# Optimization experiments

Measured on AMD Instinct MI355X. Metric: run time of the kernel, lower is better.

## Reference

```python
import jax, jax.numpy as jnp
import numpy as np

THR = 1.0  # snntorch Leaky default threshold
BETA = 0.9


def setup_inputs() -> dict:
    key = jax.random.key(0)
    k_in, k_w1, k_b1, k_w2, k_b2 = jax.random.split(key, 5)
    T, B, D, H = 100, 256, 784, 256
    # binary spike train input (rate-coded)
    spike_input = (jax.random.uniform(k_in, (T, B, D)) < 0.5).astype(jnp.float32)
    # nn.Linear init: U(-1/sqrt(fan_in), 1/sqrt(fan_in))
    lim1 = 1.0 / np.sqrt(D)
    lim2 = 1.0 / np.sqrt(H)
    W1 = jax.random.uniform(k_w1, (H, D), minval=-lim1, maxval=lim1, dtype=jnp.float32)
    b1 = jax.random.uniform(k_b1, (H,), minval=-lim1, maxval=lim1, dtype=jnp.float32)
    W2 = jax.random.uniform(k_w2, (D, H), minval=-lim2, maxval=lim2, dtype=jnp.float32)
    b2 = jax.random.uniform(k_b2, (D,), minval=-lim2, maxval=lim2, dtype=jnp.float32)
    return {"spike_input": spike_input, "W1": W1, "b1": b1, "W2": W2, "b2": b2}


def _heaviside(x):
    return (x > 0).astype(x.dtype)


def reference(spike_input, W1, b1, W2, b2):
    T, B, D = spike_input.shape
    H = W1.shape[0]

    def step(carry, x_t):
        mem1, mem2 = carry
        # layer 1: Linear + Leaky LIF (reset-by-subtraction, as in snntorch)
        cur1 = x_t @ W1.T + b1                          # [B,H]
        reset1 = _heaviside(mem1 - THR)                 # spikes from previous mem
        mem1 = BETA * mem1 + cur1 - reset1 * THR
        spk1 = _heaviside(mem1 - THR)
        # layer 2
        cur2 = spk1 @ W2.T + b2                         # [B,D]
        reset2 = _heaviside(mem2 - THR)
        mem2 = BETA * mem2 + cur2 - reset2 * THR
        spk2 = _heaviside(mem2 - THR)
        return (mem1, mem2), spk2

    mem1_0 = jnp.zeros((B, H), dtype=spike_input.dtype)
    mem2_0 = jnp.zeros((B, D), dtype=spike_input.dtype)
    _, spk_out = jax.lax.scan(step, (mem1_0, mem2_0), spike_input)
    return spk_out  # [T,B,D]
```

## Files before the change

kernel.cpp:

```cpp
#include <hip/hip_runtime.h>

typedef __attribute__((ext_vector_type(8))) _Float16 f16x8;
typedef __attribute__((ext_vector_type(4))) float f32x4;

static constexpr int TT = 100, BB = 256, DD = 784, HH = 256;
static constexpr int MM = TT * BB;
static constexpr int K1PAD = 800;
static constexpr int N2PAD = 800;
static constexpr float MIDSC = 2048.0f, INVMID = 1.0f / 2048.0f;

__device__ __forceinline__ unsigned short f2h(float x) {
  _Float16 h = (_Float16)x;
  return *(unsigned short*)&h;
}
__device__ __forceinline__ float h2f(unsigned short u) {
  _Float16 h = *(_Float16*)&u;
  return (float)h;
}
__device__ __forceinline__ void glds16(const void* g, void* l) {
  __builtin_amdgcn_global_load_lds(
      (const __attribute__((address_space(1))) unsigned int*)g,
      (__attribute__((address_space(3))) unsigned int*)l, 16, 0, 0);
}

__global__ __launch_bounds__(256)
void split_w(const float* __restrict__ W, unsigned short* __restrict__ Ws,
             int N, int K, int Npad, int Kpad) {
  int idx = blockIdx.x * 256 + threadIdx.x;
  int total = Npad * Kpad;
  if (idx >= total) return;
  int row = idx / Kpad, col = idx - row * Kpad;
  float w = (row < N && col < K) ? W[row * K + col] : 0.0f;
  unsigned short h0 = f2h(w);
  float r = (w - h2f(h0)) * MIDSC;
  Ws[idx] = h0;
  Ws[total + idx] = f2h(r);
}

__global__ __launch_bounds__(256, 2)
void gemm1(const float* __restrict__ X, const unsigned short* __restrict__ Bs,
           const float* __restrict__ bias, float* __restrict__ C) {
  constexpr int Kpad = K1PAD, nkb = Kpad / 32;
  __shared__ unsigned short Asm[2][128 * 32];
  __shared__ unsigned short Bsm[3][2][128 * 32];
  const int tid = threadIdx.x;
  const int bm = blockIdx.x * 128, bn = blockIdx.y * 128;
  const int wid = tid >> 6, lane = tid & 63;
  const int wr = (wid >> 1) * 64, wc = (wid & 1) * 64;
  const int l15 = lane & 15, l4 = lane >> 4;

  f32x4 acc[2][4][4];
#pragma unroll
  for (int s = 0; s < 2; ++s)
#pragma unroll
    for (int m = 0; m < 4; ++m)
#pragma unroll
      for (int n = 0; n < 4; ++n) acc[s][m][n] = (f32x4){0.f, 0.f, 0.f, 0.f};

  const int rl = wid * 32 + (lane >> 2);
  const int ce = ((lane & 3) ^ ((lane >> 3) & 3)) * 8;
  const size_t pstr = (size_t)HH * Kpad;
  const unsigned short* bsrc0 = Bs + (size_t)(bn + rl) * Kpad + ce;
  const unsigned short* bsrc1 = Bs + (size_t)(bn + rl + 16) * Kpad + ce;

  const int rdsw = (l4 ^ ((l15 >> 1) & 3)) * 8;

  const int r0 = tid >> 2;
  const int c0log = (tid & 3) * 8;
  const int c0phys = ((tid & 3) ^ ((tid >> 3) & 3)) * 8;

  float4 aA[4], aB[4];

  auto loadA = [&](int kb, float4 (&d)[4]) {
    const int col = kb * 32 + c0log;
    const bool ok = col < DD;
    const int colc = ok ? col : 0;
    const float* p0 = &X[(size_t)(bm + r0) * DD + colc];
    const float* p1 = &X[(size_t)(bm + r0 + 64) * DD + colc];
    d[0] = *(const float4*)p0; d[1] = *(const float4*)(p0 + 4);
    d[2] = *(const float4*)p1; d[3] = *(const float4*)(p1 + 4);
    if (!ok) {
      const float4 z = make_float4(0.f, 0.f, 0.f, 0.f);
      d[0] = z; d[1] = z; d[2] = z; d[3] = z;
    }
  };
  auto packA = [&](int bi, const float4 (&s_)[4]) {
    const unsigned ONE = 0x3C00u;
    auto pk = [&](float a, float b) {
      return (a != 0.f ? ONE : 0u) | (b != 0.f ? (ONE << 16) : 0u);
    };
    uint4 v0, v1;
    v0.x = pk(s_[0].x, s_[0].y); v0.y = pk(s_[0].z, s_[0].w);
    v0.z = pk(s_[1].x, s_[1].y); v0.w = pk(s_[1].z, s_[1].w);
    v1.x = pk(s_[2].x, s_[2].y); v1.y = pk(s_[2].z, s_[2].w);
    v1.z = pk(s_[3].x, s_[3].y); v1.w = pk(s_[3].z, s_[3].w);
    *(uint4*)&Asm[bi][r0 * 32 + c0phys] = v0;
    *(uint4*)&Asm[bi][(r0 + 64) * 32 + c0phys] = v1;
  };
  auto stageB = [&](int t) {
    const int k0 = t * 32, bi = t % 3;
    glds16(bsrc0 + k0, &Bsm[bi][0][(wid * 32) * 32]);
    glds16(bsrc1 + k0, &Bsm[bi][0][(wid * 32 + 16) * 32]);
    glds16(bsrc0 + pstr + k0, &Bsm[bi][1][(wid * 32) * 32]);
    glds16(bsrc1 + pstr + k0, &Bsm[bi][1][(wid * 32 + 16) * 32]);
  };
  auto compute = [&](int kb) {
    const int cb = kb & 1, b3 = kb % 3;
    f16x8 afr[4];
#pragma unroll
    for (int m = 0; m < 4; ++m)
      afr[m] = *(const f16x8*)&Asm[cb][(wr + m * 16 + l15) * 32 + rdsw];
#pragma unroll
    for (int s = 0; s < 2; ++s) {
      f16x8 bfr[4];
#pragma unroll
      for (int n = 0; n < 4; ++n)
        bfr[n] = *(const f16x8*)&Bsm[b3][s][(wc + n * 16 + l15) * 32 + rdsw];
#pragma unroll
      for (int m = 0; m < 4; ++m)
#pragma unroll
        for (int n = 0; n < 4; ++n)
          acc[s][m][n] = __builtin_amdgcn_mfma_f32_16x16x32_f16(afr[m], bfr[n], acc[s][m][n], 0, 0, 0);
    }
  };
  auto stepK = [&](int kb, const float4 (&pk_)[4], float4 (&ld_)[4]) {
    if (kb + 1 < nkb) packA((kb + 1) & 1, pk_);
    if (kb + 2 < nkb) stageB(kb + 2);
    compute(kb);
    __builtin_amdgcn_sched_barrier(0);
    if (kb + 2 < nkb) asm volatile("s_waitcnt vmcnt(4)" ::: "memory");
    else              asm volatile("s_waitcnt vmcnt(0)" ::: "memory");
    if (kb + 2 < nkb) loadA(kb + 2, ld_);
    asm volatile("s_waitcnt lgkmcnt(0)" ::: "memory");
    __builtin_amdgcn_sched_barrier(0);
    __builtin_amdgcn_s_barrier();
    __builtin_amdgcn_sched_barrier(0);
  };

  loadA(0, aA);
  stageB(0); stageB(1);
  asm volatile("s_waitcnt vmcnt(8)" ::: "memory");
  packA(0, aA);
  loadA(1, aB);
  asm volatile("s_waitcnt vmcnt(8)" ::: "memory");
  asm volatile("s_waitcnt lgkmcnt(0)" ::: "memory");
  __builtin_amdgcn_s_barrier();
  __builtin_amdgcn_sched_barrier(0);

  for (int kb2 = 0; kb2 < nkb; kb2 += 2) {
    stepK(kb2, aB, aA);
    if (kb2 + 1 < nkb) stepK(kb2 + 1, aA, aB);
  }

#pragma unroll
  for (int m = 0; m < 4; ++m)
#pragma unroll
    for (int n = 0; n < 4; ++n) {
      const int col = bn + wc + n * 16 + l15;
      const float bv = bias[col];
#pragma unroll
      for (int r = 0; r < 4; ++r) {
        const int row = bm + wr + m * 16 + l4 * 4 + r;
        C[(size_t)row * HH + col] = fmaf(acc[1][m][n][r], INVMID, acc[0][m][n][r]) + bv;
      }
    }
}

__global__ __launch_bounds__(256)
void lif_scan_h4(const float4* __restrict__ cur, uint2* __restrict__ spk,
                 int NE4, int nt) {
  const int tid = blockIdx.x * 256 + threadIdx.x;
  float4 mem = make_float4(0.f, 0.f, 0.f, 0.f);
  auto step1 = [](float& m, float c) {
    const float reset = (m > 1.0f) ? 1.0f : 0.0f;
    m = __fsub_rn(__fadd_rn(__fmul_rn(0.9f, m), c), reset);
    return (m > 1.0f);
  };
#pragma unroll 4
  for (int t = 0; t < nt; ++t) {
    const float4 c = cur[(size_t)t * NE4 + tid];
    unsigned s0 = step1(mem.x, c.x) ? 0x3C00u : 0u;
    unsigned s1 = step1(mem.y, c.y) ? 0x3C00u : 0u;
    unsigned s2 = step1(mem.z, c.z) ? 0x3C00u : 0u;
    unsigned s3 = step1(mem.w, c.w) ? 0x3C00u : 0u;
    uint2 o;
    o.x = s0 | (s1 << 16);
    o.y = s2 | (s3 << 16);
    spk[(size_t)t * NE4 + tid] = o;
  }
}

__global__ __launch_bounds__(64)
void fused_l2(const unsigned short* __restrict__ spk1,
              const unsigned short* __restrict__ W2s,
              const float* __restrict__ b2, float* __restrict__ out) {
  __shared__ unsigned short Asm[4][16 * 256];
  const int lane = threadIdx.x;
  const int l15 = lane & 15, l4 = lane >> 4;
  const int bb = blockIdx.x / 49, dd = blockIdx.x - bb * 49;
  const int b0 = bb * 16, d0 = dd * 16;

  const unsigned short* asrc[8];
#pragma unroll
  for (int i = 0; i < 8; ++i) {
    const int r = 2 * i + (lane >> 5);
    const int e = ((lane & 31) * 8) ^ ((r & 7) << 3);
    asrc[i] = spk1 + (size_t)(b0 + r) * HH + e;
  }
  auto stageA = [&](int t) {
    const size_t toff = (size_t)t * (BB * HH);
    unsigned short* dst = &Asm[t & 3][0];
#pragma unroll
    for (int i = 0; i < 8; ++i)
      glds16(asrc[i] + toff, dst + 2 * i * 256);
  };

  stageA(0);
  stageA(1);

  f16x8 wfr[2][8];
  const unsigned short* wb = W2s + (size_t)(d0 + l15) * HH + l4 * 8;
#pragma unroll
  for (int s = 0; s < 2; ++s)
#pragma unroll
    for (int ks = 0; ks < 8; ++ks)
      wfr[s][ks] = *(const f16x8*)(wb + (size_t)s * (N2PAD * HH) + ks * 32);
  const float bv = b2[d0 + l15];

  asm volatile("s_waitcnt vmcnt(0)" ::: "memory");
  __builtin_amdgcn_sched_barrier(0);

  f32x4 mem = (f32x4){0.f, 0.f, 0.f, 0.f};
  float* obase = out + (size_t)(b0 + l4 * 4) * DD + d0 + l15;

  for (int t = 0; t < TT; ++t) {
    if (t + 2 < TT) stageA(t + 2);
    if (t >= 2) {
      if (t <= 97)      asm volatile("s_waitcnt vmcnt(24)" ::: "memory");
      else if (t == 98) asm volatile("s_waitcnt vmcnt(16)" ::: "memory");
      else              asm volatile("s_waitcnt vmcnt(8)" ::: "memory");
    }
    __builtin_amdgcn_sched_barrier(0);

    const unsigned short* abuf = &Asm[t & 3][0];
    f32x4 p0a = (f32x4){0.f, 0.f, 0.f, 0.f}, p0b = p0a, p1a = p0a, p1b = p0a;
#pragma unroll
    for (int ks = 0; ks < 4; ++ks) {
      const f16x8 a = *(const f16x8*)&abuf[l15 * 256 + ((ks * 32 + l4 * 8) ^ ((l15 & 7) << 3))];
      p0a = __builtin_amdgcn_mfma_f32_16x16x32_f16(a, wfr[0][ks], p0a, 0, 0, 0);
      p1a = __builtin_amdgcn_mfma_f32_16x16x32_f16(a, wfr[1][ks], p1a, 0, 0, 0);
    }
#pragma unroll
    for (int ks = 4; ks < 8; ++ks) {
      const f16x8 a = *(const f16x8*)&abuf[l15 * 256 + ((ks * 32 + l4 * 8) ^ ((l15 & 7) << 3))];
      p0b = __builtin_amdgcn_mfma_f32_16x16x32_f16(a, wfr[0][ks], p0b, 0, 0, 0);
      p1b = __builtin_amdgcn_mfma_f32_16x16x32_f16(a, wfr[1][ks], p1b, 0, 0, 0);
    }

    float* op = obase + (size_t)t * ((size_t)BB * DD);
#pragma unroll
    for (int r = 0; r < 4; ++r) {
      const float p0 = p0a[r] + p0b[r];
      const float p1 = p1a[r] + p1b[r];
      const float cur = fmaf(p1, INVMID, p0) + bv;
      const float reset = (mem[r] > 1.0f) ? 1.0f : 0.0f;
      mem[r] = __fsub_rn(__fadd_rn(__fmul_rn(0.9f, mem[r]), cur), reset);
      op[(size_t)r * DD] = (mem[r] > 1.0f) ? 1.0f : 0.0f;
    }
  }
}

extern "C" void kernel_launch(void* const* d_in, const int* in_sizes, int n_in,
                              void* d_out, int out_size, void* d_ws, size_t ws_size,
                              hipStream_t stream) {
  const float* x  = (const float*)d_in[0];
  const float* W1 = (const float*)d_in[1];
  const float* b1 = (const float*)d_in[2];
  const float* W2 = (const float*)d_in[3];
  const float* b2 = (const float*)d_in[4];
  float* out = (float*)d_out;

  const size_t w1s_elems = (size_t)2 * HH * K1PAD;
  const size_t w2s_elems = (size_t)2 * N2PAD * HH;
  unsigned short* W1s = (unsigned short*)d_ws;
  unsigned short* W2s = W1s + w1s_elems;
  float* cur1 = (float*)(W2s + w2s_elems);
  unsigned short* spk1 = (unsigned short*)(cur1 + (size_t)MM * HH);

  dim3 blk(256);

  split_w<<<dim3((HH * K1PAD + 255) / 256), blk, 0, stream>>>(W1, W1s, HH, DD, HH, K1PAD);
  split_w<<<dim3((N2PAD * HH + 255) / 256), blk, 0, stream>>>(W2, W2s, DD, HH, N2PAD, HH);

  gemm1<<<dim3(MM / 128, HH / 128), blk, 0, stream>>>(x, W1s, b1, cur1);

  lif_scan_h4<<<dim3((BB * HH / 4) / 256), blk, 0, stream>>>(
      (const float4*)cur1, (uint2*)spk1, BB * HH / 4, TT);

  fused_l2<<<dim3(16 * 49), dim3(64), 0, stream>>>(spk1, W2s, b2, out);
}
```

Baseline: 110.1 us.

## Widen gemm1 tiles to full H and double fused_l2 output columns per block

```diff
diff --git a/kernel.cpp b/kernel.cpp
--- a/kernel.cpp
+++ b/kernel.cpp
@@ -37,16 +37,16 @@
   Ws[total + idx] = f2h(r);
 }
 
-__global__ __launch_bounds__(256, 2)
+__global__ __launch_bounds__(512, 2)
 void gemm1(const float* __restrict__ X, const unsigned short* __restrict__ Bs,
            const float* __restrict__ bias, float* __restrict__ C) {
   constexpr int Kpad = K1PAD, nkb = Kpad / 32;
   __shared__ unsigned short Asm[2][128 * 32];
-  __shared__ unsigned short Bsm[3][2][128 * 32];
+  __shared__ unsigned short Bsm[3][2][256 * 32];
   const int tid = threadIdx.x;
-  const int bm = blockIdx.x * 128, bn = blockIdx.y * 128;
+  const int bm = blockIdx.x * 128;
   const int wid = tid >> 6, lane = tid & 63;
-  const int wr = (wid >> 1) * 64, wc = (wid & 1) * 64;
+  const int wr = (wid >> 2) * 64, wc = (wid & 3) * 64;
   const int l15 = lane & 15, l4 = lane >> 4;
 
   f32x4 acc[2][4][4];
@@ -60,8 +60,8 @@
   const int rl = wid * 32 + (lane >> 2);
   const int ce = ((lane & 3) ^ ((lane >> 3) & 3)) * 8;
   const size_t pstr = (size_t)HH * Kpad;
-  const unsigned short* bsrc0 = Bs + (size_t)(bn + rl) * Kpad + ce;
-  const unsigned short* bsrc1 = Bs + (size_t)(bn + rl + 16) * Kpad + ce;
+  const unsigned short* bsrc0 = Bs + (size_t)rl * Kpad + ce;
+  const unsigned short* bsrc1 = Bs + (size_t)(rl + 16) * Kpad + ce;
 
   const int rdsw = (l4 ^ ((l15 >> 1) & 3)) * 8;
 
@@ -69,38 +69,33 @@
   const int c0log = (tid & 3) * 8;
   const int c0phys = ((tid & 3) ^ ((tid >> 3) & 3)) * 8;
 
-  float4 aA[4], aB[4];
-
-  auto loadA = [&](int kb, float4 (&d)[4]) {
+  float4 aA[2], aB[2];
+
+  auto loadA = [&](int kb, float4 (&d)[2]) {
     const int col = kb * 32 + c0log;
-    const bool ok = col < DD;
-    const int colc = ok ? col : 0;
-    const float* p0 = &X[(size_t)(bm + r0) * DD + colc];
-    const float* p1 = &X[(size_t)(bm + r0 + 64) * DD + colc];
-    d[0] = *(const float4*)p0; d[1] = *(const float4*)(p0 + 4);
-    d[2] = *(const float4*)p1; d[3] = *(const float4*)(p1 + 4);
-    if (!ok) {
-      const float4 z = make_float4(0.f, 0.f, 0.f, 0.f);
-      d[0] = z; d[1] = z; d[2] = z; d[3] = z;
-    }
-  };
-  auto packA = [&](int bi, const float4 (&s_)[4]) {
-    const unsigned ONE = 0x3C00u;
-    auto pk = [&](float a, float b) {
-      return (a != 0.f ? ONE : 0u) | (b != 0.f ? (ONE << 16) : 0u);
+    if (col < DD) {
+      const float* p = &X[(size_t)(bm + r0) * DD + col];
+      d[0] = *(const float4*)p;
+      d[1] = *(const float4*)(p + 4);
+    } else {
+      d[0] = make_float4(0.f, 0.f, 0.f, 0.f);
+      d[1] = d[0];
+    }
+  };
+  auto packA = [&](int bi, const float4 (&s_)[2]) {
+    auto pk = [](float a, float b) {
+      return ((__float_as_uint(a) >> 16) & 0x3C00u) |
+             (__float_as_uint(b) & 0x3C000000u);
     };
-    uint4 v0, v1;
-    v0.x = pk(s_[0].x, s_[0].y); v0.y = pk(s_[0].z, s_[0].w);
-    v0.z = pk(s_[1].x, s_[1].y); v0.w = pk(s_[1].z, s_[1].w);
-    v1.x = pk(s_[2].x, s_[2].y); v1.y = pk(s_[2].z, s_[2].w);
-    v1.z = pk(s_[3].x, s_[3].y); v1.w = pk(s_[3].z, s_[3].w);
-    *(uint4*)&Asm[bi][r0 * 32 + c0phys] = v0;
-    *(uint4*)&Asm[bi][(r0 + 64) * 32 + c0phys] = v1;
+    uint4 v;
+    v.x = pk(s_[0].x, s_[0].y); v.y = pk(s_[0].z, s_[0].w);
+    v.z = pk(s_[1].x, s_[1].y); v.w = pk(s_[1].z, s_[1].w);
+    *(uint4*)&Asm[bi][r0 * 32 + c0phys] = v;
   };
   auto stageB = [&](int t) {
     const int k0 = t * 32, bi = t % 3;
-    glds16(bsrc0 + k0, &Bsm[bi][0][(wid * 32) * 32]);
-    glds16(bsrc1 + k0, &Bsm[bi][0][(wid * 32 + 16) * 32]);
+    glds16(bsrc0 + k0,        &Bsm[bi][0][(wid * 32) * 32]);
+    glds16(bsrc1 + k0,        &Bsm[bi][0][(wid * 32 + 16) * 32]);
     glds16(bsrc0 + pstr + k0, &Bsm[bi][1][(wid * 32) * 32]);
     glds16(bsrc1 + pstr + k0, &Bsm[bi][1][(wid * 32 + 16) * 32]);
   };
@@ -123,14 +118,14 @@
           acc[s][m][n] = __builtin_amdgcn_mfma_f32_16x16x32_f16(afr[m], bfr[n], acc[s][m][n], 0, 0, 0);
     }
   };
-  auto stepK = [&](int kb, const float4 (&pk_)[4], float4 (&ld_)[4]) {
+  auto stepK = [&](int kb, const float4 (&pk_)[2], float4 (&ld_)[2]) {
+    if (kb + 2 < nkb) loadA(kb + 2, ld_);
     if (kb + 1 < nkb) packA((kb + 1) & 1, pk_);
     if (kb + 2 < nkb) stageB(kb + 2);
     compute(kb);
     __builtin_amdgcn_sched_barrier(0);
-    if (kb + 2 < nkb) asm volatile("s_waitcnt vmcnt(4)" ::: "memory");
+    if (kb + 2 < nkb) asm volatile("s_waitcnt vmcnt(6)" ::: "memory");
     else              asm volatile("s_waitcnt vmcnt(0)" ::: "memory");
-    if (kb + 2 < nkb) loadA(kb + 2, ld_);
     asm volatile("s_waitcnt lgkmcnt(0)" ::: "memory");
     __builtin_amdgcn_sched_barrier(0);
     __builtin_amdgcn_s_barrier();
@@ -138,11 +133,11 @@
   };
 
   loadA(0, aA);
-  stageB(0); stageB(1);
-  asm volatile("s_waitcnt vmcnt(8)" ::: "memory");
+  stageB(0);
+  loadA(1, aB);
+  stageB(1);
   packA(0, aA);
-  loadA(1, aB);
-  asm volatile("s_waitcnt vmcnt(8)" ::: "memory");
+  asm volatile("s_waitcnt vmcnt(6)" ::: "memory");
   asm volatile("s_waitcnt lgkmcnt(0)" ::: "memory");
   __builtin_amdgcn_s_barrier();
   __builtin_amdgcn_sched_barrier(0);
@@ -156,7 +151,7 @@
   for (int m = 0; m < 4; ++m)
 #pragma unroll
     for (int n = 0; n < 4; ++n) {
-      const int col = bn + wc + n * 16 + l15;
+      const int col = wc + n * 16 + l15;
       const float bv = bias[col];
 #pragma unroll
       for (int r = 0; r < 4; ++r) {
@@ -197,8 +192,22 @@
   __shared__ unsigned short Asm[4][16 * 256];
   const int lane = threadIdx.x;
   const int l15 = lane & 15, l4 = lane >> 4;
-  const int bb = blockIdx.x / 49, dd = blockIdx.x - bb * 49;
-  const int b0 = bb * 16, d0 = dd * 16;
+  const int bb = blockIdx.x / 25, pr = blockIdx.x - bb * 25;
+  const int b0 = bb * 16, d0 = pr * 32;
+  const bool st2 = (d0 + 16) < DD;
+
+  f16x8 w1[2][8], w2[2][8];
+  const unsigned short* wb1 = W2s + (size_t)(d0 + l15) * HH + l4 * 8;
+  const unsigned short* wb2 = W2s + (size_t)(d0 + 16 + l15) * HH + l4 * 8;
+#pragma unroll
+  for (int s = 0; s < 2; ++s)
+#pragma unroll
+    for (int ks = 0; ks < 8; ++ks) {
+      w1[s][ks] = *(const f16x8*)(wb1 + (size_t)s * (N2PAD * HH) + ks * 32);
+      w2[s][ks] = *(const f16x8*)(wb2 + (size_t)s * (N2PAD * HH) + ks * 32);
+    }
+  const float bv1 = b2[d0 + l15];
+  const float bv2 = st2 ? b2[d0 + 16 + l15] : 0.f;
 
   const unsigned short* asrc[8];
 #pragma unroll
@@ -218,54 +227,66 @@
   stageA(0);
   stageA(1);
 
-  f16x8 wfr[2][8];
-  const unsigned short* wb = W2s + (size_t)(d0 + l15) * HH + l4 * 8;
-#pragma unroll
-  for (int s = 0; s < 2; ++s)
-#pragma unroll
-    for (int ks = 0; ks < 8; ++ks)
-      wfr[s][ks] = *(const f16x8*)(wb + (size_t)s * (N2PAD * HH) + ks * 32);
-  const float bv = b2[d0 + l15];
-
-  asm volatile("s_waitcnt vmcnt(0)" ::: "memory");
-  __builtin_amdgcn_sched_barrier(0);
-
-  f32x4 mem = (f32x4){0.f, 0.f, 0.f, 0.f};
-  float* obase = out + (size_t)(b0 + l4 * 4) * DD + d0 + l15;
+  f32x4 mem1 = (f32x4){0.f, 0.f, 0.f, 0.f}, mem2 = mem1;
+  float* ob1 = out + (size_t)(b0 + l4 * 4) * DD + d0 + l15;
+  float* ob2 = ob1 + 16;
 
   for (int t = 0; t < TT; ++t) {
     if (t + 2 < TT) stageA(t + 2);
-    if (t >= 2) {
-      if (t <= 97)      asm volatile("s_waitcnt vmcnt(24)" ::: "memory");
-      else if (t == 98) asm volatile("s_waitcnt vmcnt(16)" ::: "memory");
-      else              asm volatile("s_waitcnt vmcnt(8)" ::: "memory");
+    if (t < 2) {
+      asm volatile("s_waitcnt vmcnt(16)" ::: "memory");
+    } else if (t <= 97) {
+      if (st2) asm volatile("s_waitcnt vmcnt(32)" ::: "memory");
+      else     asm volatile("s_waitcnt vmcnt(24)" ::: "memory");
+    } else if (t == 98) {
+      if (st2) asm volatile("s_waitcnt vmcnt(24)" ::: "memory");
+      else     asm volatile("s_waitcnt vmcnt(16)" ::: "memory");
+    } else {
+      if (st2) asm volatile("s_waitcnt vmcnt(16)" ::: "memory");
+      else     asm volatile("s_waitcnt vmcnt(8)" ::: "memory");
     }
     __builtin_amdgcn_sched_barrier(0);
 
     const unsigned short* abuf = &Asm[t & 3][0];
-    f32x4 p0a = (f32x4){0.f, 0.f, 0.f, 0.f}, p0b = p0a, p1a = p0a, p1b = p0a;
+    f32x4 q0a = (f32x4){0.f, 0.f, 0.f, 0.f}, q0b = q0a, q1a = q0a, q1b = q0a;
+    f32x4 u0a = q0a, u0b = q0a, u1a = q0a, u1b = q0a;
 #pragma unroll
     for (int ks = 0; ks < 4; ++ks) {
       const f16x8 a = *(const f16x8*)&abuf[l15 * 256 + ((ks * 32 + l4 * 8) ^ ((l15 & 7) << 3))];
-      p0a = __builtin_amdgcn_mfma_f32_16x16x32_f16(a, wfr[0][ks], p0a, 0, 0, 0);
-      p1a = __builtin_amdgcn_mfma_f32_16x16x32_f16(a, wfr[1][ks], p1a, 0, 0, 0);
+      q0a = __builtin_amdgcn_mfma_f32_16x16x32_f16(a, w1[0][ks], q0a, 0, 0, 0);
+      q1a = __builtin_amdgcn_mfma_f32_16x16x32_f16(a, w1[1][ks], q1a, 0, 0, 0);
+      u0a = __builtin_amdgcn_mfma_f32_16x16x32_f16(a, w2[0][ks], u0a, 0, 0, 0);
+      u1a = __builtin_amdgcn_mfma_f32_16x16x32_f16(a, w2[1][ks], u1a, 0, 0, 0);
     }
 #pragma unroll
     for (int ks = 4; ks < 8; ++ks) {
       const f16x8 a = *(const f16x8*)&abuf[l15 * 256 + ((ks * 32 + l4 * 8) ^ ((l15 & 7) << 3))];
-      p0b = __builtin_amdgcn_mfma_f32_16x16x32_f16(a, wfr[0][ks], p0b, 0, 0, 0);
-      p1b = __builtin_amdgcn_mfma_f32_16x16x32_f16(a, wfr[1][ks], p1b, 0, 0, 0);
-    }
-
-    float* op = obase + (size_t)t * ((size_t)BB * DD);
+      q0b = __builtin_amdgcn_mfma_f32_16x16x32_f16(a, w1[0][ks], q0b, 0, 0, 0);
+      q1b = __builtin_amdgcn_mfma_f32_16x16x32_f16(a, w1[1][ks], q1b, 0, 0, 0);
+      u0b = __builtin_amdgcn_mfma_f32_16x16x32_f16(a, w2[0][ks], u0b, 0, 0, 0);
+      u1b = __builtin_amdgcn_mfma_f32_16x16x32_f16(a, w2[1][ks], u1b, 0, 0, 0);
+    }
+
+    const size_t to = (size_t)t * ((size_t)BB * DD);
 #pragma unroll
     for (int r = 0; r < 4; ++r) {
-      const float p0 = p0a[r] + p0b[r];
-      const float p1 = p1a[r] + p1b[r];
-      const float cur = fmaf(p1, INVMID, p0) + bv;
-      const float reset = (mem[r] > 1.0f) ? 1.0f : 0.0f;
-      mem[r] = __fsub_rn(__fadd_rn(__fmul_rn(0.9f, mem[r]), cur), reset);
-      op[(size_t)r * DD] = (mem[r] > 1.0f) ? 1.0f : 0.0f;
+      const float p0 = q0a[r] + q0b[r];
+      const float p1 = q1a[r] + q1b[r];
+      const float cur = fmaf(p1, INVMID, p0) + bv1;
+      const float reset = (mem1[r] > 1.0f) ? 1.0f : 0.0f;
+      mem1[r] = __fsub_rn(__fadd_rn(__fmul_rn(0.9f, mem1[r]), cur), reset);
+      ob1[to + (size_t)r * DD] = (mem1[r] > 1.0f) ? 1.0f : 0.0f;
+    }
+    if (st2) {
+#pragma unroll
+      for (int r = 0; r < 4; ++r) {
+        const float p0 = u0a[r] + u0b[r];
+        const float p1 = u1a[r] + u1b[r];
+        const float cur = fmaf(p1, INVMID, p0) + bv2;
+        const float reset = (mem2[r] > 1.0f) ? 1.0f : 0.0f;
+        mem2[r] = __fsub_rn(__fadd_rn(__fmul_rn(0.9f, mem2[r]), cur), reset);
+        ob2[to + (size_t)r * DD] = (mem2[r] > 1.0f) ? 1.0f : 0.0f;
+      }
     }
   }
 }
@@ -292,10 +313,10 @@
   split_w<<<dim3((HH * K1PAD + 255) / 256), blk, 0, stream>>>(W1, W1s, HH, DD, HH, K1PAD);
   split_w<<<dim3((N2PAD * HH + 255) / 256), blk, 0, stream>>>(W2, W2s, DD, HH, N2PAD, HH);
 
-  gemm1<<<dim3(MM / 128, HH / 128), blk, 0, stream>>>(x, W1s, b1, cur1);
+  gemm1<<<dim3(MM / 128), dim3(512), 0, stream>>>(x, W1s, b1, cur1);
 
   lif_scan_h4<<<dim3((BB * HH / 4) / 256), blk, 0, stream>>>(
       (const float4*)cur1, (uint2*)spk1, BB * HH / 4, TT);
 
-  fused_l2<<<dim3(16 * 49), dim3(64), 0, stream>>>(spk1, W2s, b2, out);
-}
+  fused_l2<<<dim3(16 * 25), dim3(64), 0, stream>>>(spk1, W2s, b2, out);
+}
```

Result: slower. 159.2 us (+44.6%).

## Split layer-2 kernel into MFMA producer wave and LIF/store consumer wave

Applied to the files above, without the earlier changes.

```diff
diff --git a/kernel.cpp b/kernel.cpp
--- a/kernel.cpp
+++ b/kernel.cpp
@@ -190,82 +190,111 @@
   }
 }
 
-__global__ __launch_bounds__(64)
+__global__ __launch_bounds__(128)
 void fused_l2(const unsigned short* __restrict__ spk1,
               const unsigned short* __restrict__ W2s,
               const float* __restrict__ b2, float* __restrict__ out) {
-  __shared__ unsigned short Asm[4][16 * 256];
-  const int lane = threadIdx.x;
+  constexpr int CT = 10;
+  __shared__ unsigned short Aring[3][16 * 256];
+  __shared__ float curb[2][CT][16 * 17];
+  const int tid = threadIdx.x, wid = tid >> 6, lane = tid & 63;
   const int l15 = lane & 15, l4 = lane >> 4;
   const int bb = blockIdx.x / 49, dd = blockIdx.x - bb * 49;
   const int b0 = bb * 16, d0 = dd * 16;
 
-  const unsigned short* asrc[8];
-#pragma unroll
-  for (int i = 0; i < 8; ++i) {
-    const int r = 2 * i + (lane >> 5);
-    const int e = ((lane & 31) * 8) ^ ((r & 7) << 3);
-    asrc[i] = spk1 + (size_t)(b0 + r) * HH + e;
-  }
-  auto stageA = [&](int t) {
-    const size_t toff = (size_t)t * (BB * HH);
-    unsigned short* dst = &Asm[t & 3][0];
-#pragma unroll
-    for (int i = 0; i < 8; ++i)
-      glds16(asrc[i] + toff, dst + 2 * i * 256);
-  };
-
-  stageA(0);
-  stageA(1);
-
-  f16x8 wfr[2][8];
-  const unsigned short* wb = W2s + (size_t)(d0 + l15) * HH + l4 * 8;
-#pragma unroll
-  for (int s = 0; s < 2; ++s)
+  if (wid == 0) {
+    const unsigned short* asrc[8];
+#pragma unroll
+    for (int i = 0; i < 8; ++i) {
+      const int r = 2 * i + (lane >> 5);
+      const int e = ((lane & 31) * 8) ^ ((r & 7) << 3);
+      asrc[i] = spk1 + (size_t)(b0 + r) * HH + e;
+    }
+    auto stageA = [&](int t) {
+      const size_t toff = (size_t)t * (BB * HH);
+      unsigned short* dst = &Aring[t % 3][0];
+#pragma unroll
+      for (int i = 0; i < 8; ++i)
+        glds16(asrc[i] + toff, dst + 2 * i * 256);
+    };
+
+    stageA(0);
+    stageA(1);
+
+    f16x8 wfr[2][8];
+    const unsigned short* wb = W2s + (size_t)(d0 + l15) * HH + l4 * 8;
+#pragma unroll
+    for (int s = 0; s < 2; ++s)
+#pragma unroll
+      for (int ks = 0; ks < 8; ++ks)
+        wfr[s][ks] = *(const f16x8*)(wb + (size_t)s * (N2PAD * HH) + ks * 32);
+    const float bv = b2[d0 + l15];
+
+    asm volatile("s_waitcnt vmcnt(0)" ::: "memory");
+    __builtin_amdgcn_sched_barrier(0);
+    stageA(0 + 2 - 2);
+
+    int roff[8];
 #pragma unroll
     for (int ks = 0; ks < 8; ++ks)
-      wfr[s][ks] = *(const f16x8*)(wb + (size_t)s * (N2PAD * HH) + ks * 32);
-  const float bv = b2[d0 + l15];
-
-  asm volatile("s_waitcnt vmcnt(0)" ::: "memory");
-  __builtin_amdgcn_sched_barrier(0);
-
-  f32x4 mem = (f32x4){0.f, 0.f, 0.f, 0.f};
-  float* obase = out + (size_t)(b0 + l4 * 4) * DD + d0 + l15;
-
-  for (int t = 0; t < TT; ++t) {
-    if (t + 2 < TT) stageA(t + 2);
-    if (t >= 2) {
-      if (t <= 97)      asm volatile("s_waitcnt vmcnt(24)" ::: "memory");
-      else if (t == 98) asm volatile("s_waitcnt vmcnt(16)" ::: "memory");
-      else              asm volatile("s_waitcnt vmcnt(8)" ::: "memory");
-    }
-    __builtin_amdgcn_sched_barrier(0);
-
-    const unsigned short* abuf = &Asm[t & 3][0];
-    f32x4 p0a = (f32x4){0.f, 0.f, 0.f, 0.f}, p0b = p0a, p1a = p0a, p1b = p0a;
-#pragma unroll
-    for (int ks = 0; ks < 4; ++ks) {
-      const f16x8 a = *(const f16x8*)&abuf[l15 * 256 + ((ks * 32 + l4 * 8) ^ ((l15 & 7) << 3))];
-      p0a = __builtin_amdgcn_mfma_f32_16x16x32_f16(a, wfr[0][ks], p0a, 0, 0, 0);
-      p1a = __builtin_amdgcn_mfma_f32_16x16x32_f16(a, wfr[1][ks], p1a, 0, 0, 0);
-    }
-#pragma unroll
-    for (int ks = 4; ks < 8; ++ks) {
-      const f16x8 a = *(const f16x8*)&abuf[l15 * 256 + ((ks * 32 + l4 * 8) ^ ((l15 & 7) << 3))];
-      p0b = __builtin_amdgcn_mfma_f32_16x16x32_f16(a, wfr[0][ks], p0b, 0, 0, 0);
-      p1b = __builtin_amdgcn_mfma_f32_16x16x32_f16(a, wfr[1][ks], p1b, 0, 0, 0);
-    }
-
-    float* op = obase + (size_t)t * ((size_t)BB * DD);
-#pragma unroll
-    for (int r = 0; r < 4; ++r) {
-      const float p0 = p0a[r] + p0b[r];
-      const float p1 = p1a[r] + p1b[r];
-      const float cur = fmaf(p1, INVMID, p0) + bv;
-      const float reset = (mem[r] > 1.0f) ? 1.0f : 0.0f;
-      mem[r] = __fsub_rn(__fadd_rn(__fmul_rn(0.9f, mem[r]), cur), reset);
-      op[(size_t)r * DD] = (mem[r] > 1.0f) ? 1.0f : 0.0f;
+      roff[ks] = l15 * 256 + ((ks * 32 + l4 * 8) ^ ((l15 & 7) << 3));
+
+    for (int t = 0; t < TT; ++t) {
+      if (t + 2 < TT) stageA(t + 2);
+      if (t + 2 < TT)      asm volatile("s_waitcnt vmcnt(16)" ::: "memory");
+      else if (t + 1 < TT) asm volatile("s_waitcnt vmcnt(8)"  ::: "memory");
+      else                 asm volatile("s_waitcnt vmcnt(0)"  ::: "memory");
+      __builtin_amdgcn_sched_barrier(0);
+
+      const unsigned short* abuf = &Aring[t % 3][0];
+      f16x8 rA[8];
+#pragma unroll
+      for (int ks = 0; ks < 8; ++ks)
+        rA[ks] = *(const f16x8*)&abuf[roff[ks]];
+      f32x4 p0a = (f32x4){0.f, 0.f, 0.f, 0.f}, p0b = p0a, p1a = p0a, p1b = p0a;
+#pragma unroll
+      for (int ks = 0; ks < 4; ++ks) {
+        p0a = __builtin_amdgcn_mfma_f32_16x16x32_f16(rA[ks], wfr[0][ks], p0a, 0, 0, 0);
+        p1a = __builtin_amdgcn_mfma_f32_16x16x32_f16(rA[ks], wfr[1][ks], p1a, 0, 0, 0);
+      }
+#pragma unroll
+      for (int ks = 4; ks < 8; ++ks) {
+        p0b = __builtin_amdgcn_mfma_f32_16x16x32_f16(rA[ks], wfr[0][ks], p0b, 0, 0, 0);
+        p1b = __builtin_amdgcn_mfma_f32_16x16x32_f16(rA[ks], wfr[1][ks], p1b, 0, 0, 0);
+      }
+      float4 cv;
+      cv.x = fmaf(p1a[0] + p1b[0], INVMID, p0a[0] + p0b[0]) + bv;
+      cv.y = fmaf(p1a[1] + p1b[1], INVMID, p0a[1] + p0b[1]) + bv;
+      cv.z = fmaf(p1a[2] + p1b[2], INVMID, p0a[2] + p0b[2]) + bv;
+      cv.w = fmaf(p1a[3] + p1b[3], INVMID, p0a[3] + p0b[3]) + bv;
+      *(float4*)&curb[(t / CT) & 1][t % CT][l15 * 17 + l4 * 4] = cv;
+
+      if (t % CT == CT - 1) {
+        asm volatile("s_waitcnt lgkmcnt(0)" ::: "memory");
+        __builtin_amdgcn_sched_barrier(0);
+        __builtin_amdgcn_s_barrier();
+      }
+    }
+  } else {
+    const int cd = lane & 15, cb4 = lane >> 4;
+    float* obase = out + (size_t)(b0 + cb4 * 4) * DD + d0 + cd;
+    float mem0 = 0.f, mem1 = 0.f, mem2 = 0.f, mem3 = 0.f;
+    auto lif1 = [](float& m, float c) {
+      const float reset = (m > 1.0f) ? 1.0f : 0.0f;
+      m = __fsub_rn(__fadd_rn(__fmul_rn(0.9f, m), c), reset);
+      return (m > 1.0f) ? 1.0f : 0.0f;
+    };
+    for (int c = 0; c < TT / CT; ++c) {
+      __builtin_amdgcn_s_barrier();
+#pragma unroll
+      for (int j = 0; j < CT; ++j) {
+        const float4 cv = *(const float4*)&curb[c & 1][j][cd * 17 + cb4 * 4];
+        float* op = obase + (size_t)(c * CT + j) * ((size_t)BB * DD);
+        op[0]            = lif1(mem0, cv.x);
+        op[(size_t)DD]   = lif1(mem1, cv.y);
+        op[(size_t)2*DD] = lif1(mem2, cv.z);
+        op[(size_t)3*DD] = lif1(mem3, cv.w);
+      }
     }
   }
 }
@@ -297,5 +326,5 @@
   lif_scan_h4<<<dim3((BB * HH / 4) / 256), blk, 0, stream>>>(
       (const float4*)cur1, (uint2*)spk1, BB * HH / 4, TT);
 
-  fused_l2<<<dim3(16 * 49), dim3(64), 0, stream>>>(spk1, W2s, b2, out);
-}
+  fused_l2<<<dim3(16 * 49), dim3(128), 0, stream>>>(spk1, W2s, b2, out);
+}
```

After: 174.9 us. +58.8%, slower.
